# Kernel tuning notes

Hardware: AMD Instinct MI355X
Metric: run time of the kernel (lower is better)

The kernel has to match this reference:

```python
import jax, jax.numpy as jnp
import numpy as np

N_NODES = 100000
N_EDGES = 6400000
N_TYPES = 16
A1, A2, A3 = 5e-06, 0.0005, 1e-08


def setup_inputs() -> dict:
    key = jax.random.key(0)
    k1, k2, k3, k4, k5, k6 = jax.random.split(key, 6)
    pos = jax.random.normal(k1, (N_NODES, 2), dtype=jnp.float32)
    vel = jax.random.normal(k2, (N_NODES, 2), dtype=jnp.float32)
    p_table = jax.random.uniform(k3, (N_TYPES, 3), dtype=jnp.float32, minval=0.5, maxval=2.0)
    field = jnp.ones((N_NODES, 1), dtype=jnp.float32)
    particle_type = jax.random.randint(k4, (N_NODES,), 0, N_TYPES, dtype=jnp.int32)
    # edges without self-loops (remove_self_loops already applied)
    dst = jax.random.randint(k5, (N_EDGES,), 0, N_NODES, dtype=jnp.int32)
    off = jax.random.randint(k6, (N_EDGES,), 1, N_NODES, dtype=jnp.int32)
    src = (dst + off) % N_NODES
    edge_index = jnp.stack([dst, src], axis=0)  # [2, E], row0=dst(i), row1=src(j)
    return {"pos": pos, "vel": vel, "p_table": p_table, "field": field,
            "particle_type": particle_type, "edge_index": edge_index}


def reference(pos, vel, p_table, field, particle_type, edge_index):
    dst = edge_index[0]  # receiver i
    src = edge_index[1]  # sender j
    dp = pos[src] - pos[dst]            # bc_dpos(pos_j - pos_i), identity BC  [E,2]
    dv = vel[src] - vel[dst]            # d_pos_j - d_pos_i                   [E,2]
    params = p_table[particle_type[dst]]  # parameters_i                      [E,3]
    d2 = jnp.sum(dp * dp, axis=1, keepdims=True)  # [E,1]
    safe_d2 = jnp.where(d2 > 0, d2, 1.0)
    cohesion = params[:, 0:1] * A1 * dp
    alignment = params[:, 1:2] * A2 * dv
    separation = -params[:, 2:3] * A3 * dp / safe_d2
    msg = (separation + alignment + cohesion) * field[src]  # [E,2]
    dd_pos = jax.ops.segment_sum(msg, dst, num_segments=pos.shape[0])  # [N,2]
    return dd_pos
```

## Files before the change

kernel.cpp:

```cpp
#include <hip/hip_runtime.h>
#include <hip/hip_fp16.h>


#define BA1 5e-06f
#define BA2 0.0005f
#define BA3 1e-08f

#define NT 256
#define NTS 1024
#define NWAVE 4
#define SEPB 12288
#define WIN 256
#define WSH 8
#define SPLIT 8
#define NBMAX 512
#define CAP 28672u
#define FPS 4194304.f

__global__ void __launch_bounds__(NT)
k_pack(const float* __restrict__ pos, const float* __restrict__ vel,
       const float* __restrict__ field,
       int N, int NB, int PBLK,
       float4* __restrict__ rec16, unsigned* __restrict__ cursor) {
    int bx = blockIdx.x, tid = threadIdx.x;
    if (bx == PBLK) {
        for (int b = tid; b < NB; b += NT) cursor[b] = (unsigned)b * CAP;
        return;
    }
    int i = bx * NT + tid;
    if (i >= N) return;
    float2 p = *reinterpret_cast<const float2*>(pos + 2 * i);
    float2 v = *reinterpret_cast<const float2*>(vel + 2 * i);
    unsigned short sx = __half_as_ushort(__float2half(v.x));
    unsigned short sy = __half_as_ushort(__float2half(v.y));
    unsigned pv = (unsigned)sx | ((unsigned)sy << 16);
    rec16[i] = make_float4(p.x, p.y, __uint_as_float(pv), field[i]);
}

__global__ void __launch_bounds__(NTS)
k_scatter(const int* __restrict__ dst, const int* __restrict__ src,
          int E, int NB,
          unsigned* __restrict__ cursor,
          unsigned* __restrict__ pk) {
    __shared__ unsigned lh[NBMAX];
    __shared__ unsigned lcur[NBMAX];
    __shared__ unsigned gbase[NBMAX];
    __shared__ unsigned sbuf[SEPB];
    __shared__ unsigned short sbkt[SEPB];
    int blk = blockIdx.x, tid = threadIdx.x;
    int s = blk * SEPB, e = min(E, s + SEPB);

    for (int b = tid; b < NBMAX; b += NTS) lh[b] = 0u;
    __syncthreads();

    int k = s + 4 * tid;
    for (; k + 3 < e; k += 4 * NTS) {
        int4 d = *reinterpret_cast<const int4*>(dst + k);
        atomicAdd(&lh[d.x >> WSH], 1u);
        atomicAdd(&lh[d.y >> WSH], 1u);
        atomicAdd(&lh[d.z >> WSH], 1u);
        atomicAdd(&lh[d.w >> WSH], 1u);
    }
    {
        int rem = (e - s) & 3;
        if (tid < rem) atomicAdd(&lh[dst[e - rem + tid] >> WSH], 1u);
    }
    __syncthreads();

    for (int b = tid; b < NBMAX; b += NTS) lcur[b] = lh[b];
    __syncthreads();
    for (int o = 1; o < NBMAX; o <<= 1) {
        unsigned v0 = 0u, v1 = 0u;
        if (tid < 256) {
            v0 = (tid >= o) ? lh[tid - o] : 0u;
            v1 = (tid + 256 >= o) ? lh[tid + 256 - o] : 0u;
        }
        __syncthreads();
        if (tid < 256) {
            lh[tid] += v0;
            lh[tid + 256] += v1;
        }
        __syncthreads();
    }
    for (int b = tid; b < NBMAX; b += NTS) {
        unsigned c = lcur[b];
        unsigned ex = lh[b] - c;
        lcur[b] = ex;
        if (b < NB && c > 0u) {
            unsigned g = atomicAdd(&cursor[b], c);
            gbase[b] = g - ex;
        }
    }
    __syncthreads();

    k = s + 4 * tid;
    for (; k + 3 < e; k += 4 * NTS) {
        int4 d = *reinterpret_cast<const int4*>(dst + k);
        int4 j = *reinterpret_cast<const int4*>(src + k);
        int b0 = d.x >> WSH; unsigned r0 = atomicAdd(&lcur[b0], 1u);
        sbuf[r0] = ((unsigned)(d.x & (WIN - 1)) << 24) | (unsigned)j.x; sbkt[r0] = (unsigned short)b0;
        int b1 = d.y >> WSH; unsigned r1 = atomicAdd(&lcur[b1], 1u);
        sbuf[r1] = ((unsigned)(d.y & (WIN - 1)) << 24) | (unsigned)j.y; sbkt[r1] = (unsigned short)b1;
        int b2 = d.z >> WSH; unsigned r2 = atomicAdd(&lcur[b2], 1u);
        sbuf[r2] = ((unsigned)(d.z & (WIN - 1)) << 24) | (unsigned)j.z; sbkt[r2] = (unsigned short)b2;
        int b3 = d.w >> WSH; unsigned r3 = atomicAdd(&lcur[b3], 1u);
        sbuf[r3] = ((unsigned)(d.w & (WIN - 1)) << 24) | (unsigned)j.w; sbkt[r3] = (unsigned short)b3;
    }
    {
        int rem = (e - s) & 3;
        if (tid < rem) {
            int kk = e - rem + tid;
            int d = dst[kk];
            int b = d >> WSH; unsigned r = atomicAdd(&lcur[b], 1u);
            sbuf[r] = ((unsigned)(d & (WIN - 1)) << 24) | (unsigned)src[kk]; sbkt[r] = (unsigned short)b;
        }
    }
    __syncthreads();

    int ne = e - s;
    for (int t = tid; t < ne; t += NTS) {
        unsigned b = sbkt[t];
        unsigned idx = gbase[b] + (unsigned)t;
        if (idx < (b + 1u) * CAP)
            pk[idx] = sbuf[t];
    }
}

__global__ void __launch_bounds__(NT, 4)
k_accum(const float4* __restrict__ rec16,
        const float* __restrict__ p_table,
        const int* __restrict__ ptype,
        const unsigned* __restrict__ pk,
        const unsigned* __restrict__ cursor,
        int N,
        float* __restrict__ out) {
    __shared__ float4 wnode[WIN];
    __shared__ float4 wcoef[WIN];
    __shared__ unsigned long long acc64[NWAVE][WIN];
    int b = blockIdx.x, tid = threadIdx.x;
    int bb = b << WSH;
    int wn = min(N - bb, WIN);
    int wv = tid >> 6;

    if (tid < wn) {
        int g = bb + tid;
        float4 r = rec16[g];
        unsigned u = __float_as_uint(r.z);
        float vx = __half2float(__ushort_as_half((unsigned short)(u & 0xFFFFu)));
        float vy = __half2float(__ushort_as_half((unsigned short)(u >> 16)));
        wnode[tid] = make_float4(r.x, r.y, vx, vy);
        int ty = ptype[g];
        wcoef[tid] = make_float4(p_table[3 * ty + 0] * BA1,
                                 p_table[3 * ty + 1] * BA2,
                                 p_table[3 * ty + 2] * BA3, 0.f);
    }
    {
        unsigned long long* a = &acc64[0][0];
        for (int t = tid; t < NWAVE * WIN; t += NT) a[t] = 0ull;
    }
    __syncthreads();

    unsigned s = (unsigned)b * CAP;
    unsigned c = cursor[b] - s;
    c = (c > CAP) ? CAP : c;
    unsigned e = s + c;

#define EDGE1(PV)                                                              \
    {                                                                          \
        unsigned p_ = (PV);                                                    \
        int l_ = (int)(p_ >> 24);                                              \
        int j_ = (int)(p_ & 0xFFFFFFu);                                        \
        float4 nj_ = rec16[j_];                                                \
        unsigned u_ = __float_as_uint(nj_.z);                                  \
        float vjx_ = __half2float(__ushort_as_half((unsigned short)(u_ & 0xFFFFu))); \
        float vjy_ = __half2float(__ushort_as_half((unsigned short)(u_ >> 16))); \
        float4 w_ = wnode[l_];                                                 \
        float4 c_ = wcoef[l_];                                                 \
        float dpx_ = nj_.x - w_.x, dpy_ = nj_.y - w_.y;                        \
        float dvx_ = vjx_ - w_.z, dvy_ = vjy_ - w_.w;                          \
        float d2_ = dpx_ * dpx_ + dpy_ * dpy_;                                 \
        float sd2_ = (d2_ > 0.f) ? d2_ : 1.f;                                  \
        float cdp_ = c_.x - c_.z / sd2_;                                       \
        float mx_ = (cdp_ * dpx_ + c_.y * dvx_) * nj_.w;                       \
        float my_ = (cdp_ * dpy_ + c_.y * dvy_) * nj_.w;                       \
        long long ax_ = (long long)(int)(mx_ * FPS);                           \
        long long ay_ = (long long)(int)(my_ * FPS);                           \
        atomicAdd(&acc64[wv][l_], (unsigned long long)((ax_ << 32) + ay_));    \
    }

    unsigned stride = (unsigned)NT * SPLIT * 4u;
    for (unsigned k0 = s + ((unsigned)blockIdx.y * NT + tid) * 4u;
         k0 + 4u <= e; k0 += stride) {
        uint4 a = *reinterpret_cast<const uint4*>(pk + k0);
        EDGE1(a.x); EDGE1(a.y); EDGE1(a.z); EDGE1(a.w);
    }
    unsigned tail = c & 3u;
    if (blockIdx.y == 0 && tid < (int)tail) EDGE1(pk[e - tail + tid]);
#undef EDGE1

    __syncthreads();
    for (int l = tid; l < wn; l += NT) {
        unsigned long long T = acc64[0][l] + acc64[1][l] +
                               acc64[2][l] + acc64[3][l];
        long long Ts = (long long)T;
        int yb = (int)(unsigned)(T & 0xFFFFFFFFull);
        long long rem = Ts - (long long)yb;
        int xb = (int)(rem >> 32);
        atomicAdd(&out[2 * (bb + l) + 0], (float)xb * (1.f / FPS));
        atomicAdd(&out[2 * (bb + l) + 1], (float)yb * (1.f / FPS));
    }
}

__global__ void boids_edge_kernel(const float* __restrict__ pos,
                                  const float* __restrict__ vel,
                                  const float* __restrict__ p_table,
                                  const float* __restrict__ field,
                                  const int* __restrict__ ptype,
                                  const int* __restrict__ dst_idx,
                                  const int* __restrict__ src_idx,
                                  float* __restrict__ out,
                                  int n_edges) {
    int e = blockIdx.x * blockDim.x + threadIdx.x;
    if (e >= n_edges) return;
    int i = dst_idx[e], j = src_idx[e];
    float2 pi = *reinterpret_cast<const float2*>(pos + 2 * i);
    float2 pj = *reinterpret_cast<const float2*>(pos + 2 * j);
    float2 vi = *reinterpret_cast<const float2*>(vel + 2 * i);
    float2 vj = *reinterpret_cast<const float2*>(vel + 2 * j);
    float dpx = pj.x - pi.x, dpy = pj.y - pi.y;
    float dvx = vj.x - vi.x, dvy = vj.y - vi.y;
    int t = ptype[i];
    float p0 = p_table[3 * t + 0], p1 = p_table[3 * t + 1], p2 = p_table[3 * t + 2];
    float d2 = dpx * dpx + dpy * dpy;
    float sd2 = (d2 > 0.0f) ? d2 : 1.0f;
    float cdp = p0 * BA1 - p2 * BA3 / sd2;
    float cdv = p1 * BA2;
    float f = field[j];
    atomicAdd(&out[2 * i + 0], (cdp * dpx + cdv * dvx) * f);
    atomicAdd(&out[2 * i + 1], (cdp * dpy + cdv * dvy) * f);
}

extern "C" void kernel_launch(void* const* d_in, const int* in_sizes, int n_in,
                              void* d_out, int out_size, void* d_ws, size_t ws_size,
                              hipStream_t stream) {
    const float* pos     = (const float*)d_in[0];
    const float* vel     = (const float*)d_in[1];
    const float* p_table = (const float*)d_in[2];
    const float* field   = (const float*)d_in[3];
    const int*   ptype   = (const int*)d_in[4];
    const int*   eidx    = (const int*)d_in[5];

    int N = in_sizes[0] / 2;
    int E = in_sizes[5] / 2;
    const int* dstI = eidx;
    const int* srcI = eidx + E;
    float* out = (float*)d_out;

    int NB    = (N + WIN - 1) >> WSH;
    int NSBLK = (E + SEPB - 1) / SEPB;
    int PBLK  = (N + NT - 1) / NT;

    size_t off_rec = 0;
    size_t off_pk  = off_rec + (size_t)N * sizeof(float4);
    size_t off_cur = off_pk + (size_t)NB * CAP * 4;
    size_t need    = off_cur + (size_t)NB * 4;

    bool ok = (ws_size >= need) && (NB <= NBMAX) && (N <= (1 << 24)) &&
              ((E & 3) == 0) &&
              ((size_t)(E / (NB > 0 ? NB : 1)) * 3 / 2 + 64 <= CAP);

    if (!ok) {
        hipMemsetAsync(out, 0, (size_t)out_size * sizeof(float), stream);
        int grid = (E + NT - 1) / NT;
        boids_edge_kernel<<<grid, NT, 0, stream>>>(pos, vel, p_table, field,
                                                   ptype, dstI, srcI, out, E);
        return;
    }

    float4*   rec16  = (float4*)((char*)d_ws + off_rec);
    unsigned* pk     = (unsigned*)((char*)d_ws + off_pk);
    unsigned* cursor = (unsigned*)((char*)d_ws + off_cur);

    hipMemsetAsync(out, 0, (size_t)out_size * sizeof(float), stream);

    k_pack   <<<PBLK + 1, NT, 0, stream>>>(pos, vel, field, N, NB, PBLK,
                                           rec16, cursor);
    k_scatter<<<NSBLK, NTS, 0, stream>>>(dstI, srcI, E, NB, cursor, pk);
    dim3 agrid(NB, SPLIT);
    k_accum  <<<agrid, NT, 0, stream>>>(rec16, p_table, ptype, pk, cursor,
                                        N, out);
}
```

Before: 80.10 us.

## Fuse node packing into scatter and replace output atomics with partial slabs

Node record packing moves into extra blocks of the scatter kernel, so the separate pack launch goes away. Cursors now hold per-bucket counts reset by a small memset instead of being initialised with base offsets. The scatter loop is replaced by fixed 3-iteration register preloading of dst/src, so each int4 is read once and reused for both histogram and placement, instead of dst being loaded twice. The accumulate kernel writes per-split partial results to a workspace slab, and a new reduce kernel sums them, replacing the output memset and float atomics. This adds a kernel launch and extra slab traffic, and relies on SEPB equalling 3*4*NTS.

```diff
diff --git a/kernel.cpp b/kernel.cpp
--- a/kernel.cpp
+++ b/kernel.cpp
@@ -17,68 +17,71 @@
 #define CAP 28672u
 #define FPS 4194304.f
 
-__global__ void __launch_bounds__(NT)
-k_pack(const float* __restrict__ pos, const float* __restrict__ vel,
-       const float* __restrict__ field,
-       int N, int NB, int PBLK,
-       float4* __restrict__ rec16, unsigned* __restrict__ cursor) {
-    int bx = blockIdx.x, tid = threadIdx.x;
-    if (bx == PBLK) {
-        for (int b = tid; b < NB; b += NT) cursor[b] = (unsigned)b * CAP;
-        return;
-    }
-    int i = bx * NT + tid;
-    if (i >= N) return;
-    float2 p = *reinterpret_cast<const float2*>(pos + 2 * i);
-    float2 v = *reinterpret_cast<const float2*>(vel + 2 * i);
-    unsigned short sx = __half_as_ushort(__float2half(v.x));
-    unsigned short sy = __half_as_ushort(__float2half(v.y));
-    unsigned pv = (unsigned)sx | ((unsigned)sy << 16);
-    rec16[i] = make_float4(p.x, p.y, __uint_as_float(pv), field[i]);
-}
-
 __global__ void __launch_bounds__(NTS)
 k_scatter(const int* __restrict__ dst, const int* __restrict__ src,
-          int E, int NB,
+          const float* __restrict__ pos, const float* __restrict__ vel,
+          const float* __restrict__ field,
+          int E, int N, int NB, int NSBLK,
           unsigned* __restrict__ cursor,
-          unsigned* __restrict__ pk) {
+          unsigned* __restrict__ pk,
+          float4* __restrict__ rec16) {
+    int bx = blockIdx.x, tid = threadIdx.x;
+
+    if (bx >= NSBLK) {
+        int i = (bx - NSBLK) * NTS + tid;
+        if (i >= N) return;
+        float2 p = *reinterpret_cast<const float2*>(pos + 2 * i);
+        float2 v = *reinterpret_cast<const float2*>(vel + 2 * i);
+        unsigned short sx = __half_as_ushort(__float2half(v.x));
+        unsigned short sy = __half_as_ushort(__float2half(v.y));
+        unsigned pv = (unsigned)sx | ((unsigned)sy << 16);
+        rec16[i] = make_float4(p.x, p.y, __uint_as_float(pv), field[i]);
+        return;
+    }
+
     __shared__ unsigned lh[NBMAX];
     __shared__ unsigned lcur[NBMAX];
     __shared__ unsigned gbase[NBMAX];
     __shared__ unsigned sbuf[SEPB];
     __shared__ unsigned short sbkt[SEPB];
-    int blk = blockIdx.x, tid = threadIdx.x;
-    int s = blk * SEPB, e = min(E, s + SEPB);
+    int s = bx * SEPB, e = min(E, s + SEPB);
 
     for (int b = tid; b < NBMAX; b += NTS) lh[b] = 0u;
     __syncthreads();
 
-    int k = s + 4 * tid;
-    for (; k + 3 < e; k += 4 * NTS) {
-        int4 d = *reinterpret_cast<const int4*>(dst + k);
-        atomicAdd(&lh[d.x >> WSH], 1u);
-        atomicAdd(&lh[d.y >> WSH], 1u);
-        atomicAdd(&lh[d.z >> WSH], 1u);
-        atomicAdd(&lh[d.w >> WSH], 1u);
-    }
-    {
-        int rem = (e - s) & 3;
-        if (tid < rem) atomicAdd(&lh[dst[e - rem + tid] >> WSH], 1u);
-    }
+    int k0 = s + 4 * tid;
+    int k1 = k0 + 4 * NTS;
+    int k2 = k0 + 8 * NTS;
+    bool v0 = (k0 + 3 < e), v1 = (k1 + 3 < e), v2 = (k2 + 3 < e);
+    int4 d0, d1, d2, j0, j1, j2;
+    if (v0) { d0 = *reinterpret_cast<const int4*>(dst + k0);
+              j0 = *reinterpret_cast<const int4*>(src + k0); }
+    if (v1) { d1 = *reinterpret_cast<const int4*>(dst + k1);
+              j1 = *reinterpret_cast<const int4*>(src + k1); }
+    if (v2) { d2 = *reinterpret_cast<const int4*>(dst + k2);
+              j2 = *reinterpret_cast<const int4*>(src + k2); }
+
+#define HIST4(D)                                                               \
+    { atomicAdd(&lh[(D).x >> WSH], 1u); atomicAdd(&lh[(D).y >> WSH], 1u);      \
+      atomicAdd(&lh[(D).z >> WSH], 1u); atomicAdd(&lh[(D).w >> WSH], 1u); }
+    if (v0) HIST4(d0);
+    if (v1) HIST4(d1);
+    if (v2) HIST4(d2);
+#undef HIST4
     __syncthreads();
 
     for (int b = tid; b < NBMAX; b += NTS) lcur[b] = lh[b];
     __syncthreads();
     for (int o = 1; o < NBMAX; o <<= 1) {
-        unsigned v0 = 0u, v1 = 0u;
+        unsigned a0 = 0u, a1 = 0u;
         if (tid < 256) {
-            v0 = (tid >= o) ? lh[tid - o] : 0u;
-            v1 = (tid + 256 >= o) ? lh[tid + 256 - o] : 0u;
+            a0 = (tid >= o) ? lh[tid - o] : 0u;
+            a1 = (tid + 256 >= o) ? lh[tid + 256 - o] : 0u;
         }
         __syncthreads();
         if (tid < 256) {
-            lh[tid] += v0;
-            lh[tid + 256] += v1;
+            lh[tid] += a0;
+            lh[tid + 256] += a1;
         }
         __syncthreads();
     }
@@ -88,33 +91,30 @@
         lcur[b] = ex;
         if (b < NB && c > 0u) {
             unsigned g = atomicAdd(&cursor[b], c);
-            gbase[b] = g - ex;
+            gbase[b] = (unsigned)b * CAP + g - ex;
         }
     }
     __syncthreads();
 
-    k = s + 4 * tid;
-    for (; k + 3 < e; k += 4 * NTS) {
-        int4 d = *reinterpret_cast<const int4*>(dst + k);
-        int4 j = *reinterpret_cast<const int4*>(src + k);
-        int b0 = d.x >> WSH; unsigned r0 = atomicAdd(&lcur[b0], 1u);
-        sbuf[r0] = ((unsigned)(d.x & (WIN - 1)) << 24) | (unsigned)j.x; sbkt[r0] = (unsigned short)b0;
-        int b1 = d.y >> WSH; unsigned r1 = atomicAdd(&lcur[b1], 1u);
-        sbuf[r1] = ((unsigned)(d.y & (WIN - 1)) << 24) | (unsigned)j.y; sbkt[r1] = (unsigned short)b1;
-        int b2 = d.z >> WSH; unsigned r2 = atomicAdd(&lcur[b2], 1u);
-        sbuf[r2] = ((unsigned)(d.z & (WIN - 1)) << 24) | (unsigned)j.z; sbkt[r2] = (unsigned short)b2;
-        int b3 = d.w >> WSH; unsigned r3 = atomicAdd(&lcur[b3], 1u);
-        sbuf[r3] = ((unsigned)(d.w & (WIN - 1)) << 24) | (unsigned)j.w; sbkt[r3] = (unsigned short)b3;
-    }
-    {
-        int rem = (e - s) & 3;
-        if (tid < rem) {
-            int kk = e - rem + tid;
-            int d = dst[kk];
-            int b = d >> WSH; unsigned r = atomicAdd(&lcur[b], 1u);
-            sbuf[r] = ((unsigned)(d & (WIN - 1)) << 24) | (unsigned)src[kk]; sbkt[r] = (unsigned short)b;
-        }
-    }
+#define PLACE4(D, J)                                                           \
+    {                                                                          \
+        int b_ = (D).x >> WSH; unsigned r_ = atomicAdd(&lcur[b_], 1u);         \
+        sbuf[r_] = ((unsigned)((D).x & (WIN - 1)) << 24) | (unsigned)(J).x;    \
+        sbkt[r_] = (unsigned short)b_;                                         \
+        b_ = (D).y >> WSH; r_ = atomicAdd(&lcur[b_], 1u);                      \
+        sbuf[r_] = ((unsigned)((D).y & (WIN - 1)) << 24) | (unsigned)(J).y;    \
+        sbkt[r_] = (unsigned short)b_;                                         \
+        b_ = (D).z >> WSH; r_ = atomicAdd(&lcur[b_], 1u);                      \
+        sbuf[r_] = ((unsigned)((D).z & (WIN - 1)) << 24) | (unsigned)(J).z;    \
+        sbkt[r_] = (unsigned short)b_;                                         \
+        b_ = (D).w >> WSH; r_ = atomicAdd(&lcur[b_], 1u);                      \
+        sbuf[r_] = ((unsigned)((D).w & (WIN - 1)) << 24) | (unsigned)(J).w;    \
+        sbkt[r_] = (unsigned short)b_;                                         \
+    }
+    if (v0) PLACE4(d0, j0);
+    if (v1) PLACE4(d1, j1);
+    if (v2) PLACE4(d2, j2);
+#undef PLACE4
     __syncthreads();
 
     int ne = e - s;
@@ -132,8 +132,8 @@
         const int* __restrict__ ptype,
         const unsigned* __restrict__ pk,
         const unsigned* __restrict__ cursor,
-        int N,
-        float* __restrict__ out) {
+        int N, int PS,
+        float* __restrict__ part) {
     __shared__ float4 wnode[WIN];
     __shared__ float4 wcoef[WIN];
     __shared__ unsigned long long acc64[NWAVE][WIN];
@@ -161,7 +161,7 @@
     __syncthreads();
 
     unsigned s = (unsigned)b * CAP;
-    unsigned c = cursor[b] - s;
+    unsigned c = cursor[b];
     c = (c > CAP) ? CAP : c;
     unsigned e = s + c;
 
@@ -199,6 +199,7 @@
 #undef EDGE1
 
     __syncthreads();
+    float* slab = part + (size_t)blockIdx.y * PS;
     for (int l = tid; l < wn; l += NT) {
         unsigned long long T = acc64[0][l] + acc64[1][l] +
                                acc64[2][l] + acc64[3][l];
@@ -206,9 +207,20 @@
         int yb = (int)(unsigned)(T & 0xFFFFFFFFull);
         long long rem = Ts - (long long)yb;
         int xb = (int)(rem >> 32);
-        atomicAdd(&out[2 * (bb + l) + 0], (float)xb * (1.f / FPS));
-        atomicAdd(&out[2 * (bb + l) + 1], (float)yb * (1.f / FPS));
-    }
+        slab[2 * (bb + l) + 0] = (float)xb * (1.f / FPS);
+        slab[2 * (bb + l) + 1] = (float)yb * (1.f / FPS);
+    }
+}
+
+__global__ void __launch_bounds__(NT)
+k_reduce(const float* __restrict__ part, float* __restrict__ out,
+         int total, int PS) {
+    int i = blockIdx.x * NT + threadIdx.x;
+    if (i >= total) return;
+    float sum = 0.f;
+#pragma unroll
+    for (int y = 0; y < SPLIT; ++y) sum += part[(size_t)y * PS + i];
+    out[i] = sum;
 }
 
 __global__ void boids_edge_kernel(const float* __restrict__ pos,
@@ -258,15 +270,17 @@
 
     int NB    = (N + WIN - 1) >> WSH;
     int NSBLK = (E + SEPB - 1) / SEPB;
-    int PBLK  = (N + NT - 1) / NT;
-
-    size_t off_rec = 0;
-    size_t off_pk  = off_rec + (size_t)N * sizeof(float4);
-    size_t off_cur = off_pk + (size_t)NB * CAP * 4;
-    size_t need    = off_cur + (size_t)NB * 4;
+    int PB    = (N + NTS - 1) / NTS;
+    int PS    = NB * 2 * WIN;
+
+    size_t off_rec  = 0;
+    size_t off_pk   = off_rec + (size_t)N * sizeof(float4);
+    size_t off_cur  = off_pk + (size_t)NB * CAP * 4;
+    size_t off_part = off_cur + (size_t)NB * 4;
+    size_t need     = off_part + (size_t)SPLIT * PS * 4;
 
     bool ok = (ws_size >= need) && (NB <= NBMAX) && (N <= (1 << 24)) &&
-              ((E & 3) == 0) &&
+              ((E & 3) == 0) && (out_size == 2 * N) &&
               ((size_t)(E / (NB > 0 ? NB : 1)) * 3 / 2 + 64 <= CAP);
 
     if (!ok) {
@@ -280,13 +294,15 @@
     float4*   rec16  = (float4*)((char*)d_ws + off_rec);
     unsigned* pk     = (unsigned*)((char*)d_ws + off_pk);
     unsigned* cursor = (unsigned*)((char*)d_ws + off_cur);
-
-    hipMemsetAsync(out, 0, (size_t)out_size * sizeof(float), stream);
-
-    k_pack   <<<PBLK + 1, NT, 0, stream>>>(pos, vel, field, N, NB, PBLK,
-                                           rec16, cursor);
-    k_scatter<<<NSBLK, NTS, 0, stream>>>(dstI, srcI, E, NB, cursor, pk);
+    float*    part   = (float*)((char*)d_ws + off_part);
+
+    hipMemsetAsync(cursor, 0, (size_t)NB * 4, stream);
+
+    k_scatter<<<NSBLK + PB, NTS, 0, stream>>>(dstI, srcI, pos, vel, field,
+                                              E, N, NB, NSBLK,
+                                              cursor, pk, rec16);
     dim3 agrid(NB, SPLIT);
     k_accum  <<<agrid, NT, 0, stream>>>(rec16, p_table, ptype, pk, cursor,
-                                        N, out);
-}
+                                        N, PS, part);
+    k_reduce <<<(2 * N + NT - 1) / NT, NT, 0, stream>>>(part, out, 2 * N, PS);
+}
```

Result: faster. 75.06 us (-6.3%).
